# Performance work log

Hardware: AMD Instinct MI355X
Metric: run time of the kernel (lower is better)

The kernel has to match this reference:

```python
import jax, jax.numpy as jnp
import numpy as np

L = 4            # num_layers (experts)
D_IN = 2048
D_OUT = 2048
B = 16384        # tokens


def setup_inputs() -> dict:
    key = jax.random.key(0)
    k_x, k_idx, k_w, k_b = jax.random.split(key, 4)
    x = jax.random.normal(k_x, (B, D_IN), dtype=jnp.float32)
    layer_idx = jax.random.randint(k_idx, (B,), 0, L, dtype=jnp.int64)
    # Per-expert linear params. Torch Linear stores W as [out,in] and computes
    # x @ W.T + b; we store the equivalent [L, in, out] layout directly.
    bound = 1.0 / np.sqrt(D_IN)
    W = jax.random.uniform(k_w, (L, D_IN, D_OUT), jnp.float32, -bound, bound)
    b = jax.random.uniform(k_b, (L, D_OUT), jnp.float32, -bound, bound)
    return {"x": x, "layer_idx": layer_idx, "W": W, "b": b}


def reference(x, layer_idx, W, b):
    # Faithful to ParallelLinear.forward with layer_idx given: the
    # split -> per-group linear -> concat -> argsort-unpermute pipeline is
    # mathematically out[j] = x[j] @ W[layer_idx[j]] + b[layer_idx[j]].
    # Dense jit-friendly form: run every expert on all tokens, then select.
    all_out = jnp.einsum('bi,lio->lbo', x, W) + b[:, None, :]   # [L, B, out]
    tok = jnp.arange(x.shape[0])
    return all_out[layer_idx, tok]                              # [B, out]
```

## Files before the change

### kernel.cpp

```cpp
#include <hip/hip_runtime.h>
#include <stdint.h>

#define L_EXPERTS 4
#define D_IN  2048
#define D_OUT 2048
#define B_TOK 16384

using f32x4  = __attribute__((ext_vector_type(4))) float;
using bf16x8 = __attribute__((ext_vector_type(8))) short;

__device__ __forceinline__ uint32_t f2bf(float f) {
    union { float f; uint32_t u; } v; v.f = f;
    uint32_t u = v.u;
    return (u + 0x7fffu + ((u >> 16) & 1u)) >> 16;
}

__device__ __forceinline__ void gl_lds16(const void* g, void* l) {
    __builtin_amdgcn_global_load_lds(
        (const __attribute__((address_space(1))) void*)g,
        (__attribute__((address_space(3))) void*)l, 16, 0, 0);
}

__global__ void hist_kernel(const int* __restrict__ idx, int* __restrict__ hist) {
    __shared__ int h[L_EXPERTS];
    if (threadIdx.x < L_EXPERTS) h[threadIdx.x] = 0;
    __syncthreads();
    const int e = idx[blockIdx.x * 256 + threadIdx.x];
    atomicAdd(&h[e], 1);
    __syncthreads();
    if (threadIdx.x < L_EXPERTS)
        hist[blockIdx.x * L_EXPERTS + threadIdx.x] = h[threadIdx.x];
}

__global__ void prefix_kernel(const int* __restrict__ hist,
                              int* __restrict__ meta, int* __restrict__ bbase) {
    __shared__ int h[64][L_EXPERTS];
    __shared__ int tot[L_EXPERTS];
    const int b = threadIdx.x >> 2, e = threadIdx.x & 3;
    h[b][e] = hist[b * L_EXPERTS + e];
    __syncthreads();
    if (threadIdx.x < L_EXPERTS) {
        int s = 0;
        for (int bb = 0; bb < 64; ++bb) s += h[bb][threadIdx.x];
        tot[threadIdx.x] = s;
    }
    __syncthreads();
    if (threadIdx.x == 0) {
        int o = 0;
        for (int ee = 0; ee < L_EXPERTS; ++ee) { meta[ee] = o; o += tot[ee]; }
        meta[L_EXPERTS] = o;
    }
    if (threadIdx.x < L_EXPERTS) {
        const int ee = threadIdx.x;
        int base = 0;
        for (int e3 = 0; e3 < ee; ++e3) base += tot[e3];
        int run = base;
        for (int bb = 0; bb < 64; ++bb) {
            bbase[bb * L_EXPERTS + ee] = run;
            run += h[bb][ee];
        }
    }
}

__global__ void scatter_kernel(const int* __restrict__ idx,
                               const int* __restrict__ bbase,
                               int* __restrict__ perm) {
    __shared__ int wcnt[4][L_EXPERTS];
    __shared__ int wbase[4][L_EXPERTS];
    const int i = blockIdx.x * 256 + threadIdx.x;
    const int e = idx[i];
    const int w = threadIdx.x >> 6;
    const int lane = threadIdx.x & 63;
    const unsigned long long lt_mask = (1ull << lane) - 1ull;
    int my_off = 0;
    #pragma unroll
    for (int ee = 0; ee < L_EXPERTS; ++ee) {
        unsigned long long m = __ballot(e == ee);
        if (lane == 0) wcnt[w][ee] = __popcll(m);
        if (e == ee) my_off = __popcll(m & lt_mask);
    }
    __syncthreads();
    if (threadIdx.x < L_EXPERTS) {
        const int ee = threadIdx.x;
        int run = bbase[blockIdx.x * L_EXPERTS + ee];
        #pragma unroll
        for (int ww = 0; ww < 4; ++ww) { wbase[ww][ee] = run; run += wcnt[ww][ee]; }
    }
    __syncthreads();
    perm[wbase[w][e] + my_off] = i;
}

__global__ void gather_convert(const float* __restrict__ x,
                               const int* __restrict__ perm,
                               uint32_t* __restrict__ Ag) {
    const int j = threadIdx.x;
    for (int p = blockIdx.x; p < B_TOK; p += gridDim.x) {
        const int t = perm[p];
        const float4* src = (const float4*)(x + (size_t)t * D_IN);
        uint4* dst = (uint4*)(Ag + (size_t)p * (D_IN / 2));
        float4 v0 = src[2 * j], v1 = src[2 * j + 1];
        uint4 o;
        o.x = f2bf(v0.x) | (f2bf(v0.y) << 16);
        o.y = f2bf(v0.z) | (f2bf(v0.w) << 16);
        o.z = f2bf(v1.x) | (f2bf(v1.y) << 16);
        o.w = f2bf(v1.z) | (f2bf(v1.w) << 16);
        dst[j] = o;
    }
}

__global__ void wtrans(const float* __restrict__ W, ushort* __restrict__ Wt) {
    __shared__ float tile[64][65];
    const int l  = blockIdx.z;
    const int k0 = blockIdx.x * 64, n0 = blockIdx.y * 64;
    const float* Wl = W + (size_t)l * D_IN * D_OUT;
    ushort* Wtl = Wt + (size_t)l * D_IN * D_OUT;
    const int t = threadIdx.x;
    const int kr = t >> 4, nc = (t & 15) * 4;
    #pragma unroll
    for (int i = 0; i < 64; i += 16) {
        float4 v = *(const float4*)&Wl[(size_t)(k0 + kr + i) * D_OUT + n0 + nc];
        tile[kr + i][nc]     = v.x; tile[kr + i][nc + 1] = v.y;
        tile[kr + i][nc + 2] = v.z; tile[kr + i][nc + 3] = v.w;
    }
    __syncthreads();
    const int nr = t >> 3, kc = (t & 7) * 8;
    #pragma unroll
    for (int i = 0; i < 64; i += 32) {
        uint4 o;
        o.x = f2bf(tile[kc + 0][nr + i]) | (f2bf(tile[kc + 1][nr + i]) << 16);
        o.y = f2bf(tile[kc + 2][nr + i]) | (f2bf(tile[kc + 3][nr + i]) << 16);
        o.z = f2bf(tile[kc + 4][nr + i]) | (f2bf(tile[kc + 5][nr + i]) << 16);
        o.w = f2bf(tile[kc + 6][nr + i]) | (f2bf(tile[kc + 7][nr + i]) << 16);
        *(uint4*)&Wtl[(size_t)(n0 + nr + i) * D_IN + k0 + kc] = o;
    }
}

__global__ __launch_bounds__(512, 2)
void gemm_grouped(const ushort* __restrict__ Ag, const ushort* __restrict__ Wt,
                  const float* __restrict__ bias, const int* __restrict__ meta,
                  const int* __restrict__ perm, float* __restrict__ out) {
    __shared__ __align__(16) ushort smem[2 * 32 * 512];

    int off[L_EXPERTS + 1];
    #pragma unroll
    for (int i = 0; i <= L_EXPERTS; ++i) off[i] = meta[i];

    const int gid = blockIdx.x;
    const int nt = gid & 7;
    const int mt = gid >> 3;

    int e = -1, lt = 0, t0 = 0;
    #pragma unroll
    for (int i = 0; i < L_EXPERTS; ++i) {
        int cnt = off[i + 1] - off[i];
        int tiles = (cnt + 255) >> 8;
        if (e < 0 && mt < t0 + tiles) { e = i; lt = mt - t0; }
        t0 += tiles;
    }
    if (e < 0) return;
    const int rowbase = off[e] + lt * 256;
    const int cnt_e   = off[e + 1] - off[e];
    const int n0      = nt * 256;

    const int tid  = threadIdx.x;
    const int lane = tid & 63;
    const int w    = tid >> 6;
    const int wm   = w & 1, wn = w >> 1;
    const int l15  = lane & 15, lq = lane >> 4;

    const ushort* gp[4];
    #pragma unroll
    for (int q = 0; q < 4; ++q) {
        const int cidx = w * 4 + q;
        if (cidx < 16) {
            int row = rowbase + cidx * 16 + l15;
            if (row > B_TOK + 127) row = B_TOK + 127;
            gp[q] = Ag + (size_t)row * D_IN + lq * 8;
        } else {
            int col = n0 + (cidx - 16) * 16 + l15;
            gp[q] = Wt + ((size_t)e * D_OUT + col) * D_IN + lq * 8;
        }
    }

    f32x4 acc[8][4] = {};
    const int NK = D_IN / 32;

    #pragma unroll
    for (int q = 0; q < 4; ++q)
        gl_lds16(gp[q], &smem[(w * 4 + q) * 512]);
    __syncthreads();

    for (int k = 0; k < NK; ++k) {
        if (k + 1 < NK) {
            const int nb = (k + 1) & 1;
            #pragma unroll
            for (int q = 0; q < 4; ++q)
                gl_lds16(gp[q] + (k + 1) * 32,
                         &smem[(nb * 32 + w * 4 + q) * 512]);
        }
        const ushort* base = &smem[(k & 1) * 32 * 512];
        bf16x8 af[8], bg[4];
        #pragma unroll
        for (int i = 0; i < 8; ++i)
            af[i] = *(const bf16x8*)&base[(wm * 8 + i) * 512 + lane * 8];
        #pragma unroll
        for (int j = 0; j < 4; ++j)
            bg[j] = *(const bf16x8*)&base[(16 + wn * 4 + j) * 512 + lane * 8];
        #pragma unroll
        for (int i = 0; i < 8; ++i)
            #pragma unroll
            for (int j = 0; j < 4; ++j)
                acc[i][j] = __builtin_amdgcn_mfma_f32_16x16x32_bf16(
                    af[i], bg[j], acc[i][j], 0, 0, 0);
        __syncthreads();
    }

    float bv[4];
    #pragma unroll
    for (int j = 0; j < 4; ++j)
        bv[j] = bias[(size_t)e * D_OUT + n0 + wn * 64 + j * 16 + l15];
    #pragma unroll
    for (int i = 0; i < 8; ++i) {
        #pragma unroll
        for (int r = 0; r < 4; ++r) {
            int lr = lt * 256 + wm * 128 + i * 16 + lq * 4 + r;
            if (lr < cnt_e) {
                int tok = perm[off[e] + lr];
                float* orow = out + (size_t)tok * D_OUT + n0 + wn * 64 + l15;
                #pragma unroll
                for (int j = 0; j < 4; ++j)
                    orow[j * 16] = acc[i][j][r] + bv[j];
            }
        }
    }
}

__global__ void fallback_kernel(const float* __restrict__ x, const int* __restrict__ idx,
                                const float* __restrict__ W, const float* __restrict__ bias,
                                float* __restrict__ out) {
    __shared__ float xs[D_IN];
    const int t = blockIdx.x;
    const int e = idx[t];
    const float* xr = x + (size_t)t * D_IN;
    for (int k = threadIdx.x; k < D_IN; k += 256) xs[k] = xr[k];
    __syncthreads();
    const float* We = W + (size_t)e * D_IN * D_OUT;
    #pragma unroll 2
    for (int j = 0; j < D_OUT / 256; ++j) {
        int col = threadIdx.x + j * 256;
        float a = bias[(size_t)e * D_OUT + col];
        for (int k = 0; k < D_IN; ++k) a += xs[k] * We[(size_t)k * D_OUT + col];
        out[(size_t)t * D_OUT + col] = a;
    }
}

extern "C" void kernel_launch(void* const* d_in, const int* in_sizes, int n_in,
                              void* d_out, int out_size, void* d_ws, size_t ws_size,
                              hipStream_t stream) {
    const float* x   = (const float*)d_in[0];
    const int*   idx = (const int*)d_in[1];
    const float* W   = (const float*)d_in[2];
    const float* b   = (const float*)d_in[3];
    float* out = (float*)d_out;

    const size_t META_OFF = 0;
    const size_t PERM_OFF = 256;
    const size_t AG_OFF   = PERM_OFF + (size_t)B_TOK * 4;
    const size_t AG_BYTES = (size_t)(B_TOK + 128) * D_IN * 2;
    const size_t WT_OFF   = AG_OFF + AG_BYTES;
    const size_t WT_BYTES = (size_t)L_EXPERTS * D_IN * D_OUT * 2;
    const size_t NEED     = WT_OFF + WT_BYTES;

    if (ws_size < NEED) {
        fallback_kernel<<<B_TOK, 256, 0, stream>>>(x, idx, W, b, out);
        return;
    }

    int*      meta   = (int*)((char*)d_ws + META_OFF);
    int*      perm   = (int*)((char*)d_ws + PERM_OFF);
    int*      hist   = (int*)((char*)d_ws + AG_OFF);
    int*      bbase  = (int*)((char*)d_ws + AG_OFF + 1024);
    uint32_t* Ag     = (uint32_t*)((char*)d_ws + AG_OFF);
    ushort*   Wt     = (ushort*)((char*)d_ws + WT_OFF);

    hist_kernel   <<<64, 256, 0, stream>>>(idx, hist);
    prefix_kernel <<<1, 256, 0, stream>>>(hist, meta, bbase);
    scatter_kernel<<<64, 256, 0, stream>>>(idx, bbase, perm);
    gather_convert<<<4096, 256, 0, stream>>>(x, perm, Ag);
    wtrans        <<<dim3(32, 32, L_EXPERTS), 256, 0, stream>>>(W, Wt);
    gemm_grouped  <<<68 * 8, 512, 0, stream>>>(
        (const ushort*)Ag, Wt, b, meta, perm, out);
}
```

Before: 544.5 us.

## Fuse prefix into scatter, merge prep kernels, triple-buffer GEMM K loop

The prefix kernel is folded into the scatter kernel: each block recomputes the per-expert totals and its own prefix from the histogram, which removes one launch. The weight transpose and the activation gather/convert become a single launch with interleaved block roles, so they run concurrently. The GEMM main loop moves from a double buffer with a full syncthreads to a three-stage LDS ring. It uses explicit vmcnt waits and raw barriers, splits the A-fragment loads into two halves, and raises wave priority around the MFMA bursts. The cost is more LDS per block (96KB), which may limit occupancy to one block per CU despite launch_bounds(512,2), plus a small amount of redundant histogram summing in every scatter block.

```diff
diff --git a/kernel.cpp b/kernel.cpp
--- a/kernel.cpp
+++ b/kernel.cpp
@@ -32,106 +32,96 @@
         hist[blockIdx.x * L_EXPERTS + threadIdx.x] = h[threadIdx.x];
 }
 
-__global__ void prefix_kernel(const int* __restrict__ hist,
-                              int* __restrict__ meta, int* __restrict__ bbase) {
-    __shared__ int h[64][L_EXPERTS];
-    __shared__ int tot[L_EXPERTS];
-    const int b = threadIdx.x >> 2, e = threadIdx.x & 3;
-    h[b][e] = hist[b * L_EXPERTS + e];
-    __syncthreads();
-    if (threadIdx.x < L_EXPERTS) {
-        int s = 0;
-        for (int bb = 0; bb < 64; ++bb) s += h[bb][threadIdx.x];
-        tot[threadIdx.x] = s;
-    }
-    __syncthreads();
-    if (threadIdx.x == 0) {
-        int o = 0;
-        for (int ee = 0; ee < L_EXPERTS; ++ee) { meta[ee] = o; o += tot[ee]; }
-        meta[L_EXPERTS] = o;
-    }
-    if (threadIdx.x < L_EXPERTS) {
-        const int ee = threadIdx.x;
-        int base = 0;
-        for (int e3 = 0; e3 < ee; ++e3) base += tot[e3];
-        int run = base;
-        for (int bb = 0; bb < 64; ++bb) {
-            bbase[bb * L_EXPERTS + ee] = run;
-            run += h[bb][ee];
-        }
-    }
-}
-
-__global__ void scatter_kernel(const int* __restrict__ idx,
-                               const int* __restrict__ bbase,
-                               int* __restrict__ perm) {
+__global__ void scatter_fused(const int* __restrict__ idx,
+                              const int* __restrict__ hist,
+                              int* __restrict__ meta,
+                              int* __restrict__ perm) {
     __shared__ int wcnt[4][L_EXPERTS];
     __shared__ int wbase[4][L_EXPERTS];
+    __shared__ int tot[L_EXPERTS], pre[L_EXPERTS];
     const int i = blockIdx.x * 256 + threadIdx.x;
     const int e = idx[i];
     const int w = threadIdx.x >> 6;
     const int lane = threadIdx.x & 63;
-    const unsigned long long lt_mask = (1ull << lane) - 1ull;
+    const unsigned long long lt = (1ull << lane) - 1ull;
     int my_off = 0;
     #pragma unroll
     for (int ee = 0; ee < L_EXPERTS; ++ee) {
         unsigned long long m = __ballot(e == ee);
         if (lane == 0) wcnt[w][ee] = __popcll(m);
-        if (e == ee) my_off = __popcll(m & lt_mask);
-    }
-    __syncthreads();
+        if (e == ee) my_off = __popcll(m & lt);
+    }
     if (threadIdx.x < L_EXPERTS) {
         const int ee = threadIdx.x;
-        int run = bbase[blockIdx.x * L_EXPERTS + ee];
+        int t = 0, p = 0;
+        for (int bb = 0; bb < 64; ++bb) {
+            int h = hist[bb * L_EXPERTS + ee];
+            if (bb < (int)blockIdx.x) p += h;
+            t += h;
+        }
+        tot[ee] = t; pre[ee] = p;
+    }
+    __syncthreads();
+    if (threadIdx.x < L_EXPERTS) {
+        const int ee = threadIdx.x;
+        int base = 0;
+        for (int e2 = 0; e2 < ee; ++e2) base += tot[e2];
+        int run = base + pre[ee];
         #pragma unroll
         for (int ww = 0; ww < 4; ++ww) { wbase[ww][ee] = run; run += wcnt[ww][ee]; }
+        if (blockIdx.x == 0) {
+            meta[ee] = base;
+            if (ee == L_EXPERTS - 1) meta[L_EXPERTS] = base + tot[ee];
+        }
     }
     __syncthreads();
     perm[wbase[w][e] + my_off] = i;
 }
 
-__global__ void gather_convert(const float* __restrict__ x,
-                               const int* __restrict__ perm,
-                               uint32_t* __restrict__ Ag) {
-    const int j = threadIdx.x;
-    for (int p = blockIdx.x; p < B_TOK; p += gridDim.x) {
-        const int t = perm[p];
-        const float4* src = (const float4*)(x + (size_t)t * D_IN);
-        uint4* dst = (uint4*)(Ag + (size_t)p * (D_IN / 2));
-        float4 v0 = src[2 * j], v1 = src[2 * j + 1];
-        uint4 o;
-        o.x = f2bf(v0.x) | (f2bf(v0.y) << 16);
-        o.y = f2bf(v0.z) | (f2bf(v0.w) << 16);
-        o.z = f2bf(v1.x) | (f2bf(v1.y) << 16);
-        o.w = f2bf(v1.z) | (f2bf(v1.w) << 16);
-        dst[j] = o;
-    }
-}
-
-__global__ void wtrans(const float* __restrict__ W, ushort* __restrict__ Wt) {
-    __shared__ float tile[64][65];
-    const int l  = blockIdx.z;
-    const int k0 = blockIdx.x * 64, n0 = blockIdx.y * 64;
-    const float* Wl = W + (size_t)l * D_IN * D_OUT;
-    ushort* Wtl = Wt + (size_t)l * D_IN * D_OUT;
-    const int t = threadIdx.x;
-    const int kr = t >> 4, nc = (t & 15) * 4;
-    #pragma unroll
-    for (int i = 0; i < 64; i += 16) {
-        float4 v = *(const float4*)&Wl[(size_t)(k0 + kr + i) * D_OUT + n0 + nc];
-        tile[kr + i][nc]     = v.x; tile[kr + i][nc + 1] = v.y;
-        tile[kr + i][nc + 2] = v.z; tile[kr + i][nc + 3] = v.w;
-    }
-    __syncthreads();
-    const int nr = t >> 3, kc = (t & 7) * 8;
-    #pragma unroll
-    for (int i = 0; i < 64; i += 32) {
-        uint4 o;
-        o.x = f2bf(tile[kc + 0][nr + i]) | (f2bf(tile[kc + 1][nr + i]) << 16);
-        o.y = f2bf(tile[kc + 2][nr + i]) | (f2bf(tile[kc + 3][nr + i]) << 16);
-        o.z = f2bf(tile[kc + 4][nr + i]) | (f2bf(tile[kc + 5][nr + i]) << 16);
-        o.w = f2bf(tile[kc + 6][nr + i]) | (f2bf(tile[kc + 7][nr + i]) << 16);
-        *(uint4*)&Wtl[(size_t)(n0 + nr + i) * D_IN + k0 + kc] = o;
+__global__ void prep_fused(const float* __restrict__ x, const int* __restrict__ perm,
+                           uint32_t* __restrict__ Ag,
+                           const float* __restrict__ W, ushort* __restrict__ Wt) {
+    const int b = blockIdx.x;
+    if ((b & 1) == 0) {
+        __shared__ float tile[64][65];
+        const int tb = b >> 1;
+        const int l  = tb >> 10;
+        const int k0 = (tb & 31) * 64, n0 = ((tb >> 5) & 31) * 64;
+        const float* Wl = W + (size_t)l * D_IN * D_OUT;
+        ushort* Wtl = Wt + (size_t)l * D_IN * D_OUT;
+        const int t = threadIdx.x;
+        const int kr = t >> 4, nc = (t & 15) * 4;
+        #pragma unroll
+        for (int i = 0; i < 64; i += 16) {
+            float4 v = *(const float4*)&Wl[(size_t)(k0 + kr + i) * D_OUT + n0 + nc];
+            tile[kr + i][nc]     = v.x; tile[kr + i][nc + 1] = v.y;
+            tile[kr + i][nc + 2] = v.z; tile[kr + i][nc + 3] = v.w;
+        }
+        __syncthreads();
+        const int nr = t >> 3, kc = (t & 7) * 8;
+        #pragma unroll
+        for (int i = 0; i < 64; i += 32) {
+            uint4 o;
+            o.x = f2bf(tile[kc + 0][nr + i]) | (f2bf(tile[kc + 1][nr + i]) << 16);
+            o.y = f2bf(tile[kc + 2][nr + i]) | (f2bf(tile[kc + 3][nr + i]) << 16);
+            o.z = f2bf(tile[kc + 4][nr + i]) | (f2bf(tile[kc + 5][nr + i]) << 16);
+            o.w = f2bf(tile[kc + 6][nr + i]) | (f2bf(tile[kc + 7][nr + i]) << 16);
+            *(uint4*)&Wtl[(size_t)(n0 + nr + i) * D_IN + k0 + kc] = o;
+        }
+    } else {
+        const int j = threadIdx.x;
+        for (int p = b >> 1; p < B_TOK; p += 4096) {
+            const int t = perm[p];
+            const float4* src = (const float4*)(x + (size_t)t * D_IN);
+            uint4* dst = (uint4*)(Ag + (size_t)p * (D_IN / 2));
+            float4 v0 = src[2 * j], v1 = src[2 * j + 1];
+            uint4 o;
+            o.x = f2bf(v0.x) | (f2bf(v0.y) << 16);
+            o.y = f2bf(v0.z) | (f2bf(v0.w) << 16);
+            o.z = f2bf(v1.x) | (f2bf(v1.y) << 16);
+            o.w = f2bf(v1.z) | (f2bf(v1.w) << 16);
+            dst[j] = o;
+        }
     }
 }
 
@@ -139,7 +129,7 @@
 void gemm_grouped(const ushort* __restrict__ Ag, const ushort* __restrict__ Wt,
                   const float* __restrict__ bias, const int* __restrict__ meta,
                   const int* __restrict__ perm, float* __restrict__ out) {
-    __shared__ __align__(16) ushort smem[2 * 32 * 512];
+    __shared__ __align__(16) ushort smem[3 * 16384];
 
     int off[L_EXPERTS + 1];
     #pragma unroll
@@ -183,37 +173,69 @@
     }
 
     f32x4 acc[8][4] = {};
-    const int NK = D_IN / 32;
-
-    #pragma unroll
-    for (int q = 0; q < 4; ++q)
-        gl_lds16(gp[q], &smem[(w * 4 + q) * 512]);
-    __syncthreads();
-
-    for (int k = 0; k < NK; ++k) {
-        if (k + 1 < NK) {
-            const int nb = (k + 1) & 1;
-            #pragma unroll
-            for (int q = 0; q < 4; ++q)
-                gl_lds16(gp[q] + (k + 1) * 32,
-                         &smem[(nb * 32 + w * 4 + q) * 512]);
-        }
-        const ushort* base = &smem[(k & 1) * 32 * 512];
-        bf16x8 af[8], bg[4];
-        #pragma unroll
-        for (int i = 0; i < 8; ++i)
-            af[i] = *(const bf16x8*)&base[(wm * 8 + i) * 512 + lane * 8];
+    const int NKT = D_IN / 32;
+
+    auto STAGE = [&](int kt, ushort* buf) {
+        #pragma unroll
+        for (int q = 0; q < 4; ++q)
+            gl_lds16(gp[q] + (size_t)kt * 32, &buf[(w * 4 + q) * 512]);
+    };
+
+    auto COMPUTE = [&](const ushort* base) {
+        bf16x8 bg[4], af[4];
         #pragma unroll
         for (int j = 0; j < 4; ++j)
             bg[j] = *(const bf16x8*)&base[(16 + wn * 4 + j) * 512 + lane * 8];
         #pragma unroll
-        for (int i = 0; i < 8; ++i)
+        for (int i = 0; i < 4; ++i)
+            af[i] = *(const bf16x8*)&base[(wm * 8 + i) * 512 + lane * 8];
+        __builtin_amdgcn_s_setprio(1);
+        #pragma unroll
+        for (int i = 0; i < 4; ++i)
             #pragma unroll
             for (int j = 0; j < 4; ++j)
                 acc[i][j] = __builtin_amdgcn_mfma_f32_16x16x32_bf16(
                     af[i], bg[j], acc[i][j], 0, 0, 0);
-        __syncthreads();
-    }
+        __builtin_amdgcn_s_setprio(0);
+        #pragma unroll
+        for (int i = 0; i < 4; ++i)
+            af[i] = *(const bf16x8*)&base[(wm * 8 + 4 + i) * 512 + lane * 8];
+        __builtin_amdgcn_s_setprio(1);
+        #pragma unroll
+        for (int i = 0; i < 4; ++i)
+            #pragma unroll
+            for (int j = 0; j < 4; ++j)
+                acc[4 + i][j] = __builtin_amdgcn_mfma_f32_16x16x32_bf16(
+                    af[i], bg[j], acc[4 + i][j], 0, 0, 0);
+        __builtin_amdgcn_s_setprio(0);
+    };
+
+    ushort* b0 = smem;
+    ushort* b1 = smem + 16384;
+    ushort* b2 = smem + 32768;
+
+    STAGE(0, b0);
+    STAGE(1, b1);
+    asm volatile("s_waitcnt vmcnt(4)" ::: "memory");
+    __builtin_amdgcn_s_barrier();
+    __builtin_amdgcn_sched_barrier(0);
+
+    ushort* pc = b0;
+    ushort* pn = b1;
+    ushort* ps = b2;
+    for (int m = 0; m < NKT - 2; ++m) {
+        STAGE(m + 2, ps);
+        COMPUTE(pc);
+        asm volatile("s_waitcnt vmcnt(4)" ::: "memory");
+        __builtin_amdgcn_s_barrier();
+        __builtin_amdgcn_sched_barrier(0);
+        ushort* t = pc; pc = pn; pn = ps; ps = t;
+    }
+    COMPUTE(pc);
+    asm volatile("s_waitcnt vmcnt(0)" ::: "memory");
+    __builtin_amdgcn_s_barrier();
+    __builtin_amdgcn_sched_barrier(0);
+    COMPUTE(pn);
 
     float bv[4];
     #pragma unroll
@@ -279,15 +301,12 @@
     int*      meta   = (int*)((char*)d_ws + META_OFF);
     int*      perm   = (int*)((char*)d_ws + PERM_OFF);
     int*      hist   = (int*)((char*)d_ws + AG_OFF);
-    int*      bbase  = (int*)((char*)d_ws + AG_OFF + 1024);
     uint32_t* Ag     = (uint32_t*)((char*)d_ws + AG_OFF);
     ushort*   Wt     = (ushort*)((char*)d_ws + WT_OFF);
 
     hist_kernel   <<<64, 256, 0, stream>>>(idx, hist);
-    prefix_kernel <<<1, 256, 0, stream>>>(hist, meta, bbase);
-    scatter_kernel<<<64, 256, 0, stream>>>(idx, bbase, perm);
-    gather_convert<<<4096, 256, 0, stream>>>(x, perm, Ag);
-    wtrans        <<<dim3(32, 32, L_EXPERTS), 256, 0, stream>>>(W, Wt);
+    scatter_fused <<<64, 256, 0, stream>>>(idx, hist, meta, perm);
+    prep_fused    <<<8192, 256, 0, stream>>>(x, perm, Ag, W, Wt);
     gemm_grouped  <<<68 * 8, 512, 0, stream>>>(
         (const ushort*)Ag, Wt, b, meta, perm, out);
 }
```

New measurement: 497.9 us. 1.09x faster.
